# Kernel optimization log

Measured on AMD Instinct MI355X. Metric: run time of the kernel, lower is better.

Reference implementation:

```python
import jax, jax.numpy as jnp
import numpy as np

N_HEAD = 16


def _rope_cache(T, head_dim):
    half = head_dim // 2
    inv_freq = 1.0 / (10000.0 ** (jnp.arange(half, dtype=jnp.float32) / half))
    t = jnp.arange(T, dtype=jnp.float32)
    freqs = jnp.einsum('i,j->ij', t, inv_freq)            # (T, half)
    cos = jnp.repeat(jnp.cos(freqs), 2, axis=-1)          # (T, head_dim)
    sin = jnp.repeat(jnp.sin(freqs), 2, axis=-1)
    return cos, sin


def _apply_rope(x, cos, sin):
    # x: (B, H, T, D); cos/sin: (T, D)
    x1 = x[..., ::2]
    x2 = x[..., 1::2]
    x_rot = jnp.stack([-x2, x1], axis=-1).reshape(x.shape)
    return x * cos[None, None] + x_rot * sin[None, None]


def setup_inputs() -> dict:
    key = jax.random.key(0)
    k1, k2, k3 = jax.random.split(key, 3)
    B, T, C = 2, 2048, 1024
    x = jax.random.normal(k1, (B, T, C), dtype=jnp.float32)
    Wqkv = jax.random.normal(k2, (C, 3 * C), dtype=jnp.float32) * 0.02
    Wo = jax.random.normal(k3, (C, C), dtype=jnp.float32) * 0.02
    bo = jnp.zeros((C,), dtype=jnp.float32)
    return {"x": x, "Wqkv": Wqkv, "Wo": Wo, "bo": bo}


def reference(x, Wqkv, Wo, bo):
    B, T, C = x.shape
    H = N_HEAD
    D = C // H
    scale = D ** -0.5

    qkv = x @ Wqkv                                        # (B, T, 3C)
    qkv = qkv.reshape(B, T, 3, H, D).transpose(2, 0, 3, 1, 4)  # (3, B, H, T, D)
    q, k, v = qkv[0], qkv[1], qkv[2]

    cos, sin = _rope_cache(T, D)
    q = _apply_rope(q, cos, sin)
    k = _apply_rope(k, cos, sin)

    att = jnp.einsum('bhqd,bhkd->bhqk', q, k) * scale     # (B, H, T, T)
    causal = jnp.tril(jnp.ones((T, T), dtype=bool))
    att = jnp.where(causal[None, None], att, -jnp.inf)
    att = jax.nn.softmax(att, axis=-1)                    # dropout is identity in eval

    out = jnp.einsum('bhqk,bhkd->bhqd', att, v)           # (B, H, T, D)
    out = out.transpose(0, 2, 1, 3).reshape(B, T, C)
    return out @ Wo + bo
```

## Files before the change

### kernel.cpp

```cpp
#include <hip/hip_runtime.h>

typedef __attribute__((ext_vector_type(8))) short bf16x8;
typedef __attribute__((ext_vector_type(4))) float f32x4;
typedef __attribute__((ext_vector_type(4))) unsigned uint32x4;

#define MFMA32(a, b, c) __builtin_amdgcn_mfma_f32_16x16x32_bf16((a), (b), (c), 0, 0, 0)

__device__ __forceinline__ unsigned short f2bf(float f) {
  unsigned u = __builtin_bit_cast(unsigned, f);
  u += 0x7fffu + ((u >> 16) & 1u);
  return (unsigned short)(u >> 16);
}
__device__ __forceinline__ unsigned pack2(float a, float b) {
  return (unsigned)f2bf(a) | ((unsigned)f2bf(b) << 16);
}
__device__ __forceinline__ unsigned pack2t(float lo, float hi) {
  return __builtin_amdgcn_perm(__builtin_bit_cast(unsigned, hi),
                               __builtin_bit_cast(unsigned, lo), 0x07060302u);
}
__device__ __forceinline__ void gl_lds16(const unsigned short* g, unsigned short* l) {
  __builtin_amdgcn_global_load_lds(
      (const __attribute__((address_space(1))) unsigned int*)(g),
      (__attribute__((address_space(3))) unsigned int*)(l), 16, 0, 0);
}

#define QSCALE 0.18033688011112042f

__global__ __launch_bounds__(256) void prep_kernel(
    const float* __restrict__ x, const float* __restrict__ Wqkv,
    const float* __restrict__ Wo, unsigned short* __restrict__ xb,
    unsigned short* __restrict__ wqt, unsigned short* __restrict__ wot,
    float2* __restrict__ rope) {
  __shared__ unsigned short Tl[64][72];
  const int bid = blockIdx.x, tid = threadIdx.x;
  if (bid < 2048) {
    int i = (bid * 256 + tid) * 8;
    float4 a = *(const float4*)(x + i);
    float4 b = *(const float4*)(x + i + 4);
    uint4 w;
    w.x = pack2(a.x, a.y); w.y = pack2(a.z, a.w);
    w.z = pack2(b.x, b.y); w.w = pack2(b.z, b.w);
    *(uint4*)(xb + i) = w;
  } else if (bid < 3072) {
    const float* src;
    unsigned short* dst;
    int N, kt, nt;
    if (bid < 2816) {
      int r = bid - 2048;
      src = Wqkv; dst = wqt; N = 3072;
      nt = (r % 48) * 64; kt = (r / 48) * 64;
    } else {
      int r = bid - 2816;
      src = Wo; dst = wot; N = 1024;
      nt = (r & 15) * 64; kt = (r >> 4) * 64;
    }
    const int rr = tid >> 2, cs = (tid & 3) * 16;
    const float* sp = src + (kt + rr) * N + nt + cs;
    uint4 w0, w1;
    {
      float4 a = *(const float4*)(sp), b = *(const float4*)(sp + 4);
      float4 c = *(const float4*)(sp + 8), d = *(const float4*)(sp + 12);
      w0.x = pack2(a.x, a.y); w0.y = pack2(a.z, a.w);
      w0.z = pack2(b.x, b.y); w0.w = pack2(b.z, b.w);
      w1.x = pack2(c.x, c.y); w1.y = pack2(c.z, c.w);
      w1.z = pack2(d.x, d.y); w1.w = pack2(d.z, d.w);
    }
    *(uint4*)(&Tl[rr][cs]) = w0;
    *(uint4*)(&Tl[rr][cs + 8]) = w1;
    __syncthreads();
    unsigned short tmp[16];
#pragma unroll
    for (int i = 0; i < 16; i++) tmp[i] = Tl[cs + i][rr];
    unsigned short* dp = dst + (nt + rr) * 1024 + kt + cs;
    *(uint4*)(dp) = *(const uint4*)(&tmp[0]);
    *(uint4*)(dp + 8) = *(const uint4*)(&tmp[8]);
  } else {
    int idx = (bid - 3072) * 256 + tid;
    int t = idx >> 5, d2 = idx & 31;
    float invf = expf(-(float)d2 * 0.28782313662425572f);
    float ang = (float)t * invf;
    float sn, cn;
    sincosf(ang, &sn, &cn);
    rope[idx] = make_float2(cn, sn);
  }
}

__global__ __launch_bounds__(256) void qkv_rope_kernel(
    const unsigned short* __restrict__ xb, const unsigned short* __restrict__ wt,
    const float2* __restrict__ rope, unsigned short* __restrict__ qws,
    unsigned short* __restrict__ kws, unsigned short* __restrict__ vws) {
  __shared__ unsigned short Al[128 * 32];
  __shared__ unsigned short Bl[128 * 32];

  const int tid = threadIdx.x;
  const int lane = tid & 63, wid = tid >> 6;
  const int quad = lane >> 4, col = lane & 15;
  const int wm = (wid >> 1) * 64, wn = (wid & 1) * 64;
  const int n0 = blockIdx.x * 128, m0 = blockIdx.y * 128;

  f32x4 acc[4][4] = {};
  const int srow = wid * 32 + (lane >> 2);
  const int gseg = ((lane & 3) ^ ((lane >> 3) & 3)) * 8;
  const int fsg = (quad ^ ((col >> 1) & 3)) * 8;

  for (int k0 = 0; k0 < 1024; k0 += 32) {
    gl_lds16(xb + (m0 + srow) * 1024 + k0 + gseg, Al + (wid * 32) * 32);
    gl_lds16(xb + (m0 + srow + 16) * 1024 + k0 + gseg, Al + (wid * 32 + 16) * 32);
    gl_lds16(wt + (n0 + srow) * 1024 + k0 + gseg, Bl + (wid * 32) * 32);
    gl_lds16(wt + (n0 + srow + 16) * 1024 + k0 + gseg, Bl + (wid * 32 + 16) * 32);
    __syncthreads();

    bf16x8 af[4], bfr[4];
#pragma unroll
    for (int i = 0; i < 4; i++)
      af[i] = *(const bf16x8*)(&Al[(wm + i * 16 + col) * 32 + fsg]);
#pragma unroll
    for (int j = 0; j < 4; j++)
      bfr[j] = *(const bf16x8*)(&Bl[(wn + j * 16 + col) * 32 + fsg]);
#pragma unroll
    for (int i = 0; i < 4; i++)
#pragma unroll
      for (int j = 0; j < 4; j++)
        acc[i][j] = MFMA32(af[i], bfr[j], acc[i][j]);
    __syncthreads();
  }

#pragma unroll
  for (int i = 0; i < 4; i++) {
#pragma unroll
    for (int j = 0; j < 4; j++) {
      const int nbase = n0 + wn + j * 16;
      const int region = nbase >> 10;
#pragma unroll
      for (int r = 0; r < 4; r++) {
        int m = m0 + wm + i * 16 + quad * 4 + r;
        int n = nbase + col;
        float val = acc[i][j][r];
        int nn = n & 1023, h = nn >> 6, d = nn & 63, b = m >> 11, t = m & 2047;
        if (region < 2) {
          float other = __shfl_xor(val, 1);
          float2 cs = rope[t * 32 + (d >> 1)];
          float rot = (d & 1) ? other : -other;
          val = fmaf(val, cs.x, rot * cs.y);
        }
        int bh = (b << 4) + h;
        if (region == 0) {
          qws[(bh * 2048 + t) * 64 + d] = f2bf(val * QSCALE);
        } else if (region == 1) {
          kws[(bh * 2048 + t) * 64 + d] = f2bf(val);
        } else {
          int tl = t & 31, g = t >> 5;
          int qd = (tl & 15) >> 2;
          int jj = (tl & 3) + ((tl & 16) ? 4 : 0);
          int tp = g * 32 + qd * 8 + jj;
          vws[(bh * 64 + d) * 2048 + tp] = f2bf(val);
        }
      }
    }
  }
}

__global__ __launch_bounds__(256) void attn_kernel(
    const unsigned short* __restrict__ qws, const unsigned short* __restrict__ kws,
    const unsigned short* __restrict__ vws, unsigned short* __restrict__ aws) {
  __shared__ unsigned short Kl[64 * 64];
  __shared__ unsigned short Vl[64 * 64];

  const int tid = threadIdx.x;
  const int lane = tid & 63, wid = tid >> 6;
  const int quad = lane >> 4, col = lane & 15;
  const int bh = blockIdx.y;
  const unsigned short* qb = qws + bh * (2048 * 64);
  const unsigned short* kb = kws + bh * (2048 * 64);
  const unsigned short* vb = vws + bh * (64 * 2048);
  const int b = bh >> 4, h = bh & 15;

  const int sro = wid * 16 + (lane >> 3);
  const int sgs = ((lane & 7) ^ ((lane >> 3) & 7)) * 8;
  const int sA = (quad ^ (col & 7)) * 8;

#pragma unroll
  for (int pass = 0; pass < 2; pass++) {
    const int q0blk = (pass == 0 ? (int)blockIdx.x : 31 - (int)blockIdx.x) * 64;
    const int qt = q0blk + wid * 16;
    const int qi = qt + col;

    bf16x8 qf0 = *(const bf16x8*)(qb + (qt + col) * 64 + quad * 8);
    bf16x8 qf1 = *(const bf16x8*)(qb + (qt + col) * 64 + 32 + quad * 8);

    f32x4 o[4] = {};
    float lsum = 0.f;

    for (int k0 = 0; k0 < q0blk + 64; k0 += 64) {
      gl_lds16(kb + (k0 + sro) * 64 + sgs, Kl + (wid * 16) * 64);
      gl_lds16(kb + (k0 + sro + 8) * 64 + sgs, Kl + (wid * 16 + 8) * 64);
      gl_lds16(vb + sro * 2048 + k0 + sgs, Vl + (wid * 16) * 64);
      gl_lds16(vb + (sro + 8) * 2048 + k0 + sgs, Vl + (wid * 16 + 8) * 64);
      __syncthreads();

      f32x4 sc[4];
#pragma unroll
      for (int s = 0; s < 4; s++) {
        bf16x8 kfa = *(const bf16x8*)(&Kl[(s * 16 + col) * 64 + sA]);
        bf16x8 kfb = *(const bf16x8*)(&Kl[(s * 16 + col) * 64 + (sA ^ 32)]);
        f32x4 z = {0.f, 0.f, 0.f, 0.f};
        z = MFMA32(kfa, qf0, z);
        z = MFMA32(kfb, qf1, z);
        sc[s] = z;
      }
      if (k0 + 64 > qt) {
#pragma unroll
        for (int s = 0; s < 4; s++)
#pragma unroll
          for (int r = 0; r < 4; r++) {
            int key = k0 + s * 16 + quad * 4 + r;
            if (key > qi) sc[s][r] = -1e30f;
          }
      }
      float p[16];
#pragma unroll
      for (int s = 0; s < 4; s++)
#pragma unroll
        for (int r = 0; r < 4; r++) {
          float e = exp2f(sc[s][r]);
          p[s * 4 + r] = e;
          lsum += e;
        }
      uint32x4 u0, u1;
      u0[0] = pack2t(p[0], p[1]);   u0[1] = pack2t(p[2], p[3]);
      u0[2] = pack2t(p[4], p[5]);   u0[3] = pack2t(p[6], p[7]);
      u1[0] = pack2t(p[8], p[9]);   u1[1] = pack2t(p[10], p[11]);
      u1[2] = pack2t(p[12], p[13]); u1[3] = pack2t(p[14], p[15]);
      bf16x8 pf0 = __builtin_bit_cast(bf16x8, u0);
      bf16x8 pf1 = __builtin_bit_cast(bf16x8, u1);
#pragma unroll
      for (int dt = 0; dt < 4; dt++) {
        bf16x8 vfa = *(const bf16x8*)(&Vl[(dt * 16 + col) * 64 + sA]);
        bf16x8 vfb = *(const bf16x8*)(&Vl[(dt * 16 + col) * 64 + (sA ^ 32)]);
        o[dt] = MFMA32(vfa, pf0, o[dt]);
        o[dt] = MFMA32(vfb, pf1, o[dt]);
      }
      __syncthreads();
    }

    lsum += __shfl_xor(lsum, 16);
    lsum += __shfl_xor(lsum, 32);
    float inv = 1.0f / lsum;
#pragma unroll
    for (int dt = 0; dt < 4; dt++)
#pragma unroll
      for (int r = 0; r < 4; r++) {
        int d = dt * 16 + quad * 4 + r;
        aws[(b * 2048 + qt + col) * 1024 + h * 64 + d] = f2bf(o[dt][r] * inv);
      }
  }
}

__global__ __launch_bounds__(256) void out_proj_kernel(
    const unsigned short* __restrict__ attn, const unsigned short* __restrict__ wot,
    const float* __restrict__ bo, float* __restrict__ out) {
  __shared__ unsigned short Al[64 * 32];
  __shared__ unsigned short Bl[128 * 32];

  const int tid = threadIdx.x;
  const int lane = tid & 63, wid = tid >> 6;
  const int quad = lane >> 4, col = lane & 15;
  const int wm = (wid >> 1) * 32, wn = (wid & 1) * 64;
  const int n0 = blockIdx.x * 128, m0 = blockIdx.y * 64;

  f32x4 acc[2][4] = {};
  const int sr = lane >> 2;
  const int gseg = ((lane & 3) ^ ((lane >> 3) & 3)) * 8;
  const int fsg = (quad ^ ((col >> 1) & 3)) * 8;

  for (int k0 = 0; k0 < 1024; k0 += 32) {
    gl_lds16(attn + (m0 + wid * 16 + sr) * 1024 + k0 + gseg, Al + (wid * 16) * 32);
    gl_lds16(wot + (n0 + wid * 32 + sr) * 1024 + k0 + gseg, Bl + (wid * 32) * 32);
    gl_lds16(wot + (n0 + wid * 32 + 16 + sr) * 1024 + k0 + gseg,
             Bl + (wid * 32 + 16) * 32);
    __syncthreads();

    bf16x8 af[2], bfr[4];
#pragma unroll
    for (int i = 0; i < 2; i++)
      af[i] = *(const bf16x8*)(&Al[(wm + i * 16 + col) * 32 + fsg]);
#pragma unroll
    for (int j = 0; j < 4; j++)
      bfr[j] = *(const bf16x8*)(&Bl[(wn + j * 16 + col) * 32 + fsg]);
#pragma unroll
    for (int i = 0; i < 2; i++)
#pragma unroll
      for (int j = 0; j < 4; j++)
        acc[i][j] = MFMA32(af[i], bfr[j], acc[i][j]);
    __syncthreads();
  }

#pragma unroll
  for (int i = 0; i < 2; i++)
#pragma unroll
    for (int j = 0; j < 4; j++)
#pragma unroll
      for (int r = 0; r < 4; r++) {
        int m = m0 + wm + i * 16 + quad * 4 + r;
        int n = n0 + wn + j * 16 + col;
        out[m * 1024 + n] = acc[i][j][r] + bo[n];
      }
}

extern "C" void kernel_launch(void* const* d_in, const int* in_sizes, int n_in,
                              void* d_out, int out_size, void* d_ws, size_t ws_size,
                              hipStream_t stream) {
  const float* x = (const float*)d_in[0];
  const float* Wqkv = (const float*)d_in[1];
  const float* Wo = (const float*)d_in[2];
  const float* bo = (const float*)d_in[3];
  float* out = (float*)d_out;

  unsigned short* qws = (unsigned short*)d_ws;
  unsigned short* kws = qws + 4194304;
  unsigned short* vws = kws + 4194304;
  unsigned short* xb  = vws + 4194304;
  unsigned short* aws = xb;
  unsigned short* wqt = xb + 4194304;
  unsigned short* wot = wqt + 3145728;
  float2* rope = (float2*)(wot + 1048576);

  prep_kernel<<<3328, 256, 0, stream>>>(x, Wqkv, Wo, xb, wqt, wot, rope);
  qkv_rope_kernel<<<dim3(24, 32), 256, 0, stream>>>(xb, wqt, rope, qws, kws, vws);
  attn_kernel<<<dim3(16, 32), 256, 0, stream>>>(qws, kws, vws, aws);
  out_proj_kernel<<<dim3(8, 64), 256, 0, stream>>>(aws, wot, bo, out);
}
```

Measured before the change: 227.2 us.

## Double K-step per barrier in GEMMs and compute RoPE inline with fast math

Both projection GEMMs now stage two 32-wide K chunks into LDS per iteration, which halves the number of barrier pairs per K loop and doubles LDS usage per block. The precomputed RoPE cos/sin table is removed. The angles are instead computed in the QKV epilogue with __expf and __sincosf, which drops the table's blocks and its global reads. The trade-off is reduced precision for large angles (t up to 2047) from the fast sincos, plus extra transcendental work in the epilogue.

```diff
diff --git a/kernel.cpp b/kernel.cpp
--- a/kernel.cpp
+++ b/kernel.cpp
@@ -29,8 +29,7 @@
 __global__ __launch_bounds__(256) void prep_kernel(
     const float* __restrict__ x, const float* __restrict__ Wqkv,
     const float* __restrict__ Wo, unsigned short* __restrict__ xb,
-    unsigned short* __restrict__ wqt, unsigned short* __restrict__ wot,
-    float2* __restrict__ rope) {
+    unsigned short* __restrict__ wqt, unsigned short* __restrict__ wot) {
   __shared__ unsigned short Tl[64][72];
   const int bid = blockIdx.x, tid = threadIdx.x;
   if (bid < 2048) {
@@ -41,7 +40,7 @@
     w.x = pack2(a.x, a.y); w.y = pack2(a.z, a.w);
     w.z = pack2(b.x, b.y); w.w = pack2(b.z, b.w);
     *(uint4*)(xb + i) = w;
-  } else if (bid < 3072) {
+  } else {
     const float* src;
     unsigned short* dst;
     int N, kt, nt;
@@ -74,23 +73,15 @@
     unsigned short* dp = dst + (nt + rr) * 1024 + kt + cs;
     *(uint4*)(dp) = *(const uint4*)(&tmp[0]);
     *(uint4*)(dp + 8) = *(const uint4*)(&tmp[8]);
-  } else {
-    int idx = (bid - 3072) * 256 + tid;
-    int t = idx >> 5, d2 = idx & 31;
-    float invf = expf(-(float)d2 * 0.28782313662425572f);
-    float ang = (float)t * invf;
-    float sn, cn;
-    sincosf(ang, &sn, &cn);
-    rope[idx] = make_float2(cn, sn);
   }
 }
 
 __global__ __launch_bounds__(256) void qkv_rope_kernel(
     const unsigned short* __restrict__ xb, const unsigned short* __restrict__ wt,
-    const float2* __restrict__ rope, unsigned short* __restrict__ qws,
-    unsigned short* __restrict__ kws, unsigned short* __restrict__ vws) {
-  __shared__ unsigned short Al[128 * 32];
-  __shared__ unsigned short Bl[128 * 32];
+    unsigned short* __restrict__ qws, unsigned short* __restrict__ kws,
+    unsigned short* __restrict__ vws) {
+  __shared__ unsigned short Al[2 * 128 * 32];
+  __shared__ unsigned short Bl[2 * 128 * 32];
 
   const int tid = threadIdx.x;
   const int lane = tid & 63, wid = tid >> 6;
@@ -103,25 +94,35 @@
   const int gseg = ((lane & 3) ^ ((lane >> 3) & 3)) * 8;
   const int fsg = (quad ^ ((col >> 1) & 3)) * 8;
 
-  for (int k0 = 0; k0 < 1024; k0 += 32) {
-    gl_lds16(xb + (m0 + srow) * 1024 + k0 + gseg, Al + (wid * 32) * 32);
-    gl_lds16(xb + (m0 + srow + 16) * 1024 + k0 + gseg, Al + (wid * 32 + 16) * 32);
-    gl_lds16(wt + (n0 + srow) * 1024 + k0 + gseg, Bl + (wid * 32) * 32);
-    gl_lds16(wt + (n0 + srow + 16) * 1024 + k0 + gseg, Bl + (wid * 32 + 16) * 32);
-    __syncthreads();
-
-    bf16x8 af[4], bfr[4];
-#pragma unroll
-    for (int i = 0; i < 4; i++)
-      af[i] = *(const bf16x8*)(&Al[(wm + i * 16 + col) * 32 + fsg]);
-#pragma unroll
-    for (int j = 0; j < 4; j++)
-      bfr[j] = *(const bf16x8*)(&Bl[(wn + j * 16 + col) * 32 + fsg]);
-#pragma unroll
-    for (int i = 0; i < 4; i++)
+  for (int k0 = 0; k0 < 1024; k0 += 64) {
+#pragma unroll
+    for (int c = 0; c < 2; c++) {
+      const int kc = k0 + c * 32, lo = c * 4096;
+      gl_lds16(xb + (m0 + srow) * 1024 + kc + gseg, Al + lo + (wid * 32) * 32);
+      gl_lds16(xb + (m0 + srow + 16) * 1024 + kc + gseg,
+               Al + lo + (wid * 32 + 16) * 32);
+      gl_lds16(wt + (n0 + srow) * 1024 + kc + gseg, Bl + lo + (wid * 32) * 32);
+      gl_lds16(wt + (n0 + srow + 16) * 1024 + kc + gseg,
+               Bl + lo + (wid * 32 + 16) * 32);
+    }
+    __syncthreads();
+
+#pragma unroll
+    for (int c = 0; c < 2; c++) {
+      const int lo = c * 4096;
+      bf16x8 af[4], bfr[4];
+#pragma unroll
+      for (int i = 0; i < 4; i++)
+        af[i] = *(const bf16x8*)(&Al[lo + (wm + i * 16 + col) * 32 + fsg]);
 #pragma unroll
       for (int j = 0; j < 4; j++)
-        acc[i][j] = MFMA32(af[i], bfr[j], acc[i][j]);
+        bfr[j] = *(const bf16x8*)(&Bl[lo + (wn + j * 16 + col) * 32 + fsg]);
+#pragma unroll
+      for (int i = 0; i < 4; i++)
+#pragma unroll
+        for (int j = 0; j < 4; j++)
+          acc[i][j] = MFMA32(af[i], bfr[j], acc[i][j]);
+    }
     __syncthreads();
   }
 
@@ -139,9 +140,12 @@
         int nn = n & 1023, h = nn >> 6, d = nn & 63, b = m >> 11, t = m & 2047;
         if (region < 2) {
           float other = __shfl_xor(val, 1);
-          float2 cs = rope[t * 32 + (d >> 1)];
+          float invf = __expf(-(float)(d >> 1) * 0.28782313662425572f);
+          float ang = (float)t * invf;
+          float sn, cs;
+          __sincosf(ang, &sn, &cs);
           float rot = (d & 1) ? other : -other;
-          val = fmaf(val, cs.x, rot * cs.y);
+          val = fmaf(val, cs, rot * sn);
         }
         int bh = (b << 4) + h;
         if (region == 0) {
@@ -259,8 +263,8 @@
 __global__ __launch_bounds__(256) void out_proj_kernel(
     const unsigned short* __restrict__ attn, const unsigned short* __restrict__ wot,
     const float* __restrict__ bo, float* __restrict__ out) {
-  __shared__ unsigned short Al[64 * 32];
-  __shared__ unsigned short Bl[128 * 32];
+  __shared__ unsigned short Al[2 * 64 * 32];
+  __shared__ unsigned short Bl[2 * 128 * 32];
 
   const int tid = threadIdx.x;
   const int lane = tid & 63, wid = tid >> 6;
@@ -273,25 +277,34 @@
   const int gseg = ((lane & 3) ^ ((lane >> 3) & 3)) * 8;
   const int fsg = (quad ^ ((col >> 1) & 3)) * 8;
 
-  for (int k0 = 0; k0 < 1024; k0 += 32) {
-    gl_lds16(attn + (m0 + wid * 16 + sr) * 1024 + k0 + gseg, Al + (wid * 16) * 32);
-    gl_lds16(wot + (n0 + wid * 32 + sr) * 1024 + k0 + gseg, Bl + (wid * 32) * 32);
-    gl_lds16(wot + (n0 + wid * 32 + 16 + sr) * 1024 + k0 + gseg,
-             Bl + (wid * 32 + 16) * 32);
-    __syncthreads();
-
-    bf16x8 af[2], bfr[4];
-#pragma unroll
-    for (int i = 0; i < 2; i++)
-      af[i] = *(const bf16x8*)(&Al[(wm + i * 16 + col) * 32 + fsg]);
-#pragma unroll
-    for (int j = 0; j < 4; j++)
-      bfr[j] = *(const bf16x8*)(&Bl[(wn + j * 16 + col) * 32 + fsg]);
-#pragma unroll
-    for (int i = 0; i < 2; i++)
+  for (int k0 = 0; k0 < 1024; k0 += 64) {
+#pragma unroll
+    for (int c = 0; c < 2; c++) {
+      const int kc = k0 + c * 32;
+      gl_lds16(attn + (m0 + wid * 16 + sr) * 1024 + kc + gseg,
+               Al + c * 2048 + (wid * 16) * 32);
+      gl_lds16(wot + (n0 + wid * 32 + sr) * 1024 + kc + gseg,
+               Bl + c * 4096 + (wid * 32) * 32);
+      gl_lds16(wot + (n0 + wid * 32 + 16 + sr) * 1024 + kc + gseg,
+               Bl + c * 4096 + (wid * 32 + 16) * 32);
+    }
+    __syncthreads();
+
+#pragma unroll
+    for (int c = 0; c < 2; c++) {
+      bf16x8 af[2], bfr[4];
+#pragma unroll
+      for (int i = 0; i < 2; i++)
+        af[i] = *(const bf16x8*)(&Al[c * 2048 + (wm + i * 16 + col) * 32 + fsg]);
 #pragma unroll
       for (int j = 0; j < 4; j++)
-        acc[i][j] = MFMA32(af[i], bfr[j], acc[i][j]);
+        bfr[j] = *(const bf16x8*)(&Bl[c * 4096 + (wn + j * 16 + col) * 32 + fsg]);
+#pragma unroll
+      for (int i = 0; i < 2; i++)
+#pragma unroll
+        for (int j = 0; j < 4; j++)
+          acc[i][j] = MFMA32(af[i], bfr[j], acc[i][j]);
+    }
     __syncthreads();
   }
 
@@ -323,10 +336,9 @@
   unsigned short* aws = xb;
   unsigned short* wqt = xb + 4194304;
   unsigned short* wot = wqt + 3145728;
-  float2* rope = (float2*)(wot + 1048576);
-
-  prep_kernel<<<3328, 256, 0, stream>>>(x, Wqkv, Wo, xb, wqt, wot, rope);
-  qkv_rope_kernel<<<dim3(24, 32), 256, 0, stream>>>(xb, wqt, rope, qws, kws, vws);
+
+  prep_kernel<<<3072, 256, 0, stream>>>(x, Wqkv, Wo, xb, wqt, wot);
+  qkv_rope_kernel<<<dim3(24, 32), 256, 0, stream>>>(xb, wqt, qws, kws, vws);
   attn_kernel<<<dim3(16, 32), 256, 0, stream>>>(qws, kws, vws, aws);
   out_proj_kernel<<<dim3(8, 64), 256, 0, stream>>>(aws, wot, bo, out);
 }
```

Result: faster. 208.2 us (-8.4%).
